# Performance work log

Hardware: AMD Instinct MI355X
Metric: run time of the kernel (lower is better)

The kernel has to match this reference:

```python
import jax, jax.numpy as jnp
import numpy as np

TOP_K = 2
NUM_EXPERTS = 8


def setup_inputs() -> dict:
    key = jax.random.key(0)
    ks = jax.random.split(key, 9)
    ob, ib, slen, dim, hidden, E = 1, 1, 2048, 2048, 1024, NUM_EXPERTS
    std = 0.02  # trunc_normal init std in the original module
    return {
        "x": jax.random.normal(ks[0], (ob, ib, slen, dim), dtype=jnp.float32),
        "gate": jax.random.normal(ks[1], (dim, E), dtype=jnp.float32) * std,
        "expert_bias": jnp.zeros((E,), dtype=jnp.float32),
        "w1": jax.random.normal(ks[2], (E, hidden, dim), dtype=jnp.float32) * std,
        "w2": jax.random.normal(ks[3], (E, dim, hidden), dtype=jnp.float32) * std,
        "w3": jax.random.normal(ks[4], (E, hidden, dim), dtype=jnp.float32) * std,
        "sw1": jax.random.normal(ks[5], (hidden, dim), dtype=jnp.float32) * std,
        "sw2": jax.random.normal(ks[6], (dim, hidden), dtype=jnp.float32) * std,
        "sw3": jax.random.normal(ks[7], (hidden, dim), dtype=jnp.float32) * std,
    }


def reference(x, gate, expert_bias, w1, w2, w3, sw1, sw2, sw3):
    ob, ib, slen, dim = x.shape
    E = w1.shape[0]
    xt = x.reshape(ob, ib * slen, dim)  # (ob, N, dim)

    # ---- router: sigmoid scores, top-k on (scores + expert_bias), gather raw scores ----
    logits = jnp.einsum('ond,de->one', xt, gate).astype(jnp.float32)
    scores = jax.nn.sigmoid(logits)                          # (ob, N, E)
    _, idx = jax.lax.top_k(scores + expert_bias, TOP_K)      # (ob, N, K) int32
    top_scores = jnp.take_along_axis(scores, idx, axis=2)    # route_norm=False, route_scale=1.0

    # combine weights: per-(token, expert) routing score (0 if not selected)
    cw = jnp.einsum('onke,onk->eon',
                    jax.nn.one_hot(idx, E, dtype=top_scores.dtype), top_scores)

    # ---- grouped experts (bf16 SwiGLU); score applied BEFORE experts ----
    # Matmul is linear, so silu(W1 @ (s*x)) == silu(s * (W1 @ x)); tokens with s=0 contribute 0.
    xb = xt.astype(jnp.bfloat16)
    s = cw[..., None].astype(jnp.bfloat16)                   # (E, ob, N, 1)
    g = jnp.einsum('ond,ehd->eonh', xb, w1.astype(jnp.bfloat16))
    u = jnp.einsum('ond,ehd->eonh', xb, w3.astype(jnp.bfloat16))
    h = jax.nn.silu(s * g) * (s * u)                         # (E, ob, N, hidden)
    routed = jnp.einsum('eonh,edh->ond', h, w2.astype(jnp.bfloat16)).astype(xt.dtype)

    # ---- shared expert (fp32 SwiGLU) ----
    hs = jax.nn.silu(jnp.einsum('ond,hd->onh', xt, sw1)) * jnp.einsum('ond,hd->onh', xt, sw3)
    shared = jnp.einsum('onh,dh->ond', hs, sw2)

    return (shared + routed).reshape(ob, ib, slen, dim)
```

## Files before the change

### kernel.cpp

```cpp
#include <hip/hip_runtime.h>

#define NTOK 2048
#define DIM  2048
#define HID  1024
#define NEXP 8
#define SHBASE 5120

typedef float f32x4 __attribute__((ext_vector_type(4)));
typedef __bf16 bf16x8 __attribute__((ext_vector_type(8)));

__device__ __forceinline__ unsigned int f2bf(float f) {
    unsigned int u = __float_as_uint(f);
    u += 0x7FFFu + ((u >> 16) & 1u);
    return u >> 16;
}
__device__ __forceinline__ float bf2f(unsigned int h) {
    return __uint_as_float(h << 16);
}
__device__ __forceinline__ int pack2(float a, float b) {
    return (int)(f2bf(a) | (f2bf(b) << 16));
}
__device__ __forceinline__ void gload16(const void* g, void* l) {
    __builtin_amdgcn_global_load_lds(
        (__attribute__((address_space(1))) void*)(g),
        (__attribute__((address_space(3))) void*)(l), 16, 0, 0);
}

__global__ __launch_bounds__(256) void cast_kernel(
    const float* __restrict__ src, unsigned short* __restrict__ dst, int n4)
{
    int i = blockIdx.x * 256 + threadIdx.x;
    if (i >= n4) return;
    float4 v = reinterpret_cast<const float4*>(src)[i];
    int2 o;
    o.x = pack2(v.x, v.y);
    o.y = pack2(v.z, v.w);
    reinterpret_cast<int2*>(dst)[i] = o;
}

__global__ __launch_bounds__(256) void router_kernel(
    const float* __restrict__ x, const float* __restrict__ gate,
    const float* __restrict__ bias, float* __restrict__ sc, int* __restrict__ top2)
{
    const int n = blockIdx.x;
    const int t = threadIdx.x;
    float acc[8];
#pragma unroll
    for (int e = 0; e < 8; ++e) acc[e] = 0.f;
    const float* xr = x + (size_t)n * DIM;
    for (int d = t; d < DIM; d += 256) {
        float xv = xr[d];
        float4 g0 = *reinterpret_cast<const float4*>(gate + d * 8);
        float4 g1 = *reinterpret_cast<const float4*>(gate + d * 8 + 4);
        acc[0] += xv * g0.x; acc[1] += xv * g0.y;
        acc[2] += xv * g0.z; acc[3] += xv * g0.w;
        acc[4] += xv * g1.x; acc[5] += xv * g1.y;
        acc[6] += xv * g1.z; acc[7] += xv * g1.w;
    }
#pragma unroll
    for (int e = 0; e < 8; ++e) {
#pragma unroll
        for (int off = 32; off > 0; off >>= 1)
            acc[e] += __shfl_down(acc[e], off, 64);
    }
    __shared__ float red[4][8];
    const int lane = t & 63, wv = t >> 6;
    if (lane == 0) {
#pragma unroll
        for (int e = 0; e < 8; ++e) red[wv][e] = acc[e];
    }
    __syncthreads();
    if (t == 0) {
        float scv[8];
#pragma unroll
        for (int e = 0; e < 8; ++e) {
            float v = red[0][e] + red[1][e] + red[2][e] + red[3][e];
            scv[e] = 1.f / (1.f + expf(-v));
        }
        int i1 = 0; float b1 = -1e30f;
#pragma unroll
        for (int e = 0; e < 8; ++e) { float b = scv[e] + bias[e]; if (b > b1) { b1 = b; i1 = e; } }
        int i2 = -1; float b2 = -1e30f;
#pragma unroll
        for (int e = 0; e < 8; ++e) { if (e == i1) continue; float b = scv[e] + bias[e]; if (b > b2) { b2 = b; i2 = e; } }
#pragma unroll
        for (int e = 0; e < 8; ++e) sc[n * 8 + e] = scv[e];
        top2[n * 2]     = i1;
        top2[n * 2 + 1] = i2;
    }
}

__global__ __launch_bounds__(256) void lists_kernel(
    const int* __restrict__ top2, int* __restrict__ gcnt, int* __restrict__ gbase,
    int* __restrict__ tid, int* __restrict__ rows)
{
    __shared__ int cnt[8], run[8], base[8];
    const int t = threadIdx.x;
    if (t < 8) { cnt[t] = 0; run[t] = 0; }
    __syncthreads();
    for (int tok = t; tok < NTOK; tok += 256) {
        atomicAdd(&cnt[top2[tok * 2]], 1);
        atomicAdd(&cnt[top2[tok * 2 + 1]], 1);
    }
    __syncthreads();
    if (t == 0) {
        int c = 0;
        for (int e = 0; e < 8; ++e) { base[e] = c; c += (cnt[e] + 127) & ~127; }
    }
    __syncthreads();
    for (int tok = t; tok < NTOK; tok += 256) {
#pragma unroll
        for (int k = 0; k < 2; ++k) {
            int e = top2[tok * 2 + k];
            int pos = atomicAdd(&run[e], 1);
            tid[e * NTOK + pos] = tok;
            rows[tok * 2 + k] = base[e] + pos;
        }
    }
    __syncthreads();
    if (t < 8) { gcnt[t] = cnt[t]; gbase[t] = base[t]; }
}

__global__ __launch_bounds__(256) void up_kernel(
    const unsigned short* __restrict__ xb,
    const unsigned short* __restrict__ w1b, const unsigned short* __restrict__ w3b,
    const unsigned short* __restrict__ sw1b, const unsigned short* __restrict__ sw3b,
    const float* __restrict__ sc, const int* __restrict__ gcnt, const int* __restrict__ gbase,
    const int* __restrict__ tid, unsigned short* __restrict__ h2g)
{
    const int e = blockIdx.z;
    int cnt, base;
    const unsigned short *w1e, *w3e;
    const int* tl = nullptr;
    if (e < NEXP) {
        cnt = gcnt[e];
        if ((int)blockIdx.x * 128 >= cnt) return;
        base = gbase[e];
        w1e = w1b + (size_t)e * HID * DIM;
        w3e = w3b + (size_t)e * HID * DIM;
        tl = tid + e * NTOK;
    } else {
        cnt = NTOK; base = SHBASE; w1e = sw1b; w3e = sw3b;
    }
    const int m0 = blockIdx.x * 128, n0 = blockIdx.y * 64;

    __shared__ char lA[16384];
    __shared__ char lB1[8192];
    __shared__ char lB2[8192];

    const int t = threadIdx.x;
    const int lane = t & 63, wv = t >> 6;
    const int wm = wv >> 1, wn = wv & 1;
    const int lr = lane & 15, hi = lane >> 4;
    const int srow = lane >> 3;
    const int scolb = (lane & 7) << 4;

    const char* aS[4]; char* aD[4];
#pragma unroll
    for (int p = 0; p < 4; ++p) {
        int r = p * 32 + wv * 8 + srow;
        int ridx = (e < NEXP) ? tl[min(m0 + r, cnt - 1)] : (m0 + r);
        aS[p] = (const char*)xb + (size_t)ridx * (DIM * 2) + (scolb ^ ((r & 7) << 4));
        aD[p] = lA + p * 4096 + wv * 1024;
    }
    const char *b1S[2], *b3S[2]; char *bD[2];
#pragma unroll
    for (int q = 0; q < 2; ++q) {
        int r = q * 32 + wv * 8 + srow;
        size_t ro = (size_t)(n0 + r) * (DIM * 2) + (scolb ^ ((r & 7) << 4));
        b1S[q] = (const char*)w1e + ro;
        b3S[q] = (const char*)w3e + ro;
        bD[q] = (char*)0 + q * 4096 + wv * 1024;
    }

    f32x4 accG[4][2], accU[4][2];
    const f32x4 zz = {0.f, 0.f, 0.f, 0.f};
#pragma unroll
    for (int m = 0; m < 4; ++m)
#pragma unroll
        for (int n = 0; n < 2; ++n) { accG[m][n] = zz; accU[m][n] = zz; }

    for (int kb = 0; kb < DIM * 2; kb += 128) {
#pragma unroll
        for (int p = 0; p < 4; ++p) gload16(aS[p] + kb, aD[p]);
#pragma unroll
        for (int q = 0; q < 2; ++q) {
            size_t off = q * 4096 + wv * 1024;
            gload16(b1S[q] + kb, lB1 + off);
            gload16(b3S[q] + kb, lB2 + off);
        }
        __syncthreads();
#pragma unroll
        for (int kk = 0; kk < 2; ++kk) {
            bf16x8 af[4], b1f[2], b2f[2];
            const int cb = kk * 64 + hi * 16;
#pragma unroll
            for (int m = 0; m < 4; ++m) {
                int row = wm * 64 + m * 16 + lr;
                af[m] = *reinterpret_cast<const bf16x8*>(lA + row * 128 + (cb ^ ((row & 7) << 4)));
            }
#pragma unroll
            for (int n = 0; n < 2; ++n) {
                int row = wn * 32 + n * 16 + lr;
                int off = row * 128 + (cb ^ ((row & 7) << 4));
                b1f[n] = *reinterpret_cast<const bf16x8*>(lB1 + off);
                b2f[n] = *reinterpret_cast<const bf16x8*>(lB2 + off);
            }
#pragma unroll
            for (int m = 0; m < 4; ++m)
#pragma unroll
                for (int n = 0; n < 2; ++n) {
                    accG[m][n] = __builtin_amdgcn_mfma_f32_16x16x32_bf16(af[m], b1f[n], accG[m][n], 0, 0, 0);
                    accU[m][n] = __builtin_amdgcn_mfma_f32_16x16x32_bf16(af[m], b2f[n], accU[m][n], 0, 0, 0);
                }
        }
        __syncthreads();
    }

#pragma unroll
    for (int m = 0; m < 4; ++m) {
#pragma unroll
        for (int r = 0; r < 4; ++r) {
            int row = wm * 64 + m * 16 + hi * 4 + r;
            float sv = 1.0f;
            if (e < NEXP) {
                int tok = tl[min(m0 + row, cnt - 1)];
                sv = sc[tok * NEXP + e];
            }
            unsigned short* hrow = h2g + (size_t)(base + m0 + row) * HID + n0;
#pragma unroll
            for (int n = 0; n < 2; ++n) {
                int col = wn * 32 + n * 16 + lr;
                float g = bf2f(f2bf(accG[m][n][r] * sv));
                float u = bf2f(f2bf(accU[m][n][r] * sv));
                float hval = (g / (1.f + __expf(-g))) * u;
                hrow[col] = (unsigned short)f2bf(hval);
            }
        }
    }
}

__global__ __launch_bounds__(256) void down_kernel(
    const unsigned short* __restrict__ h2g,
    const unsigned short* __restrict__ w2b, const unsigned short* __restrict__ sw2b,
    const int* __restrict__ gcnt, const int* __restrict__ gbase,
    unsigned short* __restrict__ rb, float* __restrict__ out)
{
    const int e = blockIdx.z;
    int cnt, base;
    const unsigned short* w2e;
    if (e < NEXP) {
        cnt = gcnt[e];
        if ((int)blockIdx.x * 128 >= cnt) return;
        base = gbase[e];
        w2e = w2b + (size_t)e * DIM * HID;
    } else {
        cnt = NTOK; base = SHBASE; w2e = sw2b;
    }
    const int m0 = blockIdx.x * 128, n0 = blockIdx.y * 128;

    __shared__ char lA[16384];
    __shared__ char lB[16384];

    const int t = threadIdx.x;
    const int lane = t & 63, wv = t >> 6;
    const int wm = wv >> 1, wn = wv & 1;
    const int lr = lane & 15, hi = lane >> 4;
    const int srow = lane >> 3;
    const int scolb = (lane & 7) << 4;

    const char* aS[4]; const char* bS[4];
#pragma unroll
    for (int p = 0; p < 4; ++p) {
        int r = p * 32 + wv * 8 + srow;
        aS[p] = (const char*)h2g + (size_t)(base + m0 + r) * (HID * 2) + (scolb ^ ((r & 7) << 4));
        bS[p] = (const char*)w2e + (size_t)(n0 + r) * (HID * 2) + (scolb ^ ((r & 7) << 4));
    }

    f32x4 acc[4][4];
    const f32x4 zz = {0.f, 0.f, 0.f, 0.f};
#pragma unroll
    for (int m = 0; m < 4; ++m)
#pragma unroll
        for (int n = 0; n < 4; ++n) acc[m][n] = zz;

    for (int kb = 0; kb < HID * 2; kb += 128) {
#pragma unroll
        for (int p = 0; p < 4; ++p) {
            size_t off = p * 4096 + wv * 1024;
            gload16(aS[p] + kb, lA + off);
            gload16(bS[p] + kb, lB + off);
        }
        __syncthreads();
#pragma unroll
        for (int kk = 0; kk < 2; ++kk) {
            bf16x8 af[4], bfr[4];
            const int cb = kk * 64 + hi * 16;
#pragma unroll
            for (int m = 0; m < 4; ++m) {
                int row = wm * 64 + m * 16 + lr;
                af[m] = *reinterpret_cast<const bf16x8*>(lA + row * 128 + (cb ^ ((row & 7) << 4)));
                int rowb = wn * 64 + m * 16 + lr;
                bfr[m] = *reinterpret_cast<const bf16x8*>(lB + rowb * 128 + (cb ^ ((rowb & 7) << 4)));
            }
#pragma unroll
            for (int m = 0; m < 4; ++m)
#pragma unroll
                for (int n = 0; n < 4; ++n)
                    acc[m][n] = __builtin_amdgcn_mfma_f32_16x16x32_bf16(af[m], bfr[n], acc[m][n], 0, 0, 0);
        }
        __syncthreads();
    }

#pragma unroll
    for (int m = 0; m < 4; ++m)
#pragma unroll
        for (int r = 0; r < 4; ++r) {
            int row = wm * 64 + m * 16 + hi * 4 + r;
            if (e < NEXP) {
                unsigned short* rrow = rb + (size_t)(base + m0 + row) * DIM + n0 + wn * 64;
#pragma unroll
                for (int n = 0; n < 4; ++n)
                    rrow[n * 16 + lr] = (unsigned short)f2bf(acc[m][n][r]);
            } else {
                float* orow = out + (size_t)(m0 + row) * DIM + n0 + wn * 64;
#pragma unroll
                for (int n = 0; n < 4; ++n)
                    orow[n * 16 + lr] = acc[m][n][r];
            }
        }
}

__global__ __launch_bounds__(256) void combine_kernel(
    const int* __restrict__ rows, const unsigned short* __restrict__ rb,
    float* __restrict__ out)
{
    int i = blockIdx.x * 256 + threadIdx.x;
    int tok = i >> 8, g = i & 255;
    int r1 = rows[tok * 2], r2 = rows[tok * 2 + 1];
    float4* op = reinterpret_cast<float4*>(out + (size_t)tok * DIM + g * 8);
    int4 a = *reinterpret_cast<const int4*>(rb + (size_t)r1 * DIM + g * 8);
    int4 b = *reinterpret_cast<const int4*>(rb + (size_t)r2 * DIM + g * 8);
    float4 o0 = op[0], o1 = op[1];
    o0.x += bf2f((unsigned)a.x & 0xFFFF) + bf2f((unsigned)b.x & 0xFFFF);
    o0.y += bf2f((unsigned)a.x >> 16)    + bf2f((unsigned)b.x >> 16);
    o0.z += bf2f((unsigned)a.y & 0xFFFF) + bf2f((unsigned)b.y & 0xFFFF);
    o0.w += bf2f((unsigned)a.y >> 16)    + bf2f((unsigned)b.y >> 16);
    o1.x += bf2f((unsigned)a.z & 0xFFFF) + bf2f((unsigned)b.z & 0xFFFF);
    o1.y += bf2f((unsigned)a.z >> 16)    + bf2f((unsigned)b.z >> 16);
    o1.z += bf2f((unsigned)a.w & 0xFFFF) + bf2f((unsigned)b.w & 0xFFFF);
    o1.w += bf2f((unsigned)a.w >> 16)    + bf2f((unsigned)b.w >> 16);
    op[0] = o0; op[1] = o1;
}

extern "C" void kernel_launch(void* const* d_in, const int* in_sizes, int n_in,
                              void* d_out, int out_size, void* d_ws, size_t ws_size,
                              hipStream_t stream) {
    const float* x    = (const float*)d_in[0];
    const float* gate = (const float*)d_in[1];
    const float* bias = (const float*)d_in[2];
    const float* w1   = (const float*)d_in[3];
    const float* w2   = (const float*)d_in[4];
    const float* w3   = (const float*)d_in[5];
    const float* sw1  = (const float*)d_in[6];
    const float* sw2  = (const float*)d_in[7];
    const float* sw3  = (const float*)d_in[8];
    float* out = (float*)d_out;

    char* ws = (char*)d_ws;
    size_t o = 0;
    unsigned short* xb   = (unsigned short*)(ws + o); o += 8388608;
    unsigned short* w1b  = (unsigned short*)(ws + o); o += 33554432;
    unsigned short* w3b  = (unsigned short*)(ws + o); o += 33554432;
    unsigned short* w2b  = (unsigned short*)(ws + o); o += 33554432;
    unsigned short* sw1b = (unsigned short*)(ws + o); o += 4194304;
    unsigned short* sw3b = (unsigned short*)(ws + o); o += 4194304;
    unsigned short* sw2b = (unsigned short*)(ws + o); o += 4194304;
    unsigned short* h2g  = (unsigned short*)(ws + o); o += 14680064;
    unsigned short* rb   = (unsigned short*)(ws + o); o += 20971520;
    float* sc            = (float*)(ws + o);          o += 65536;
    int* top2            = (int*)(ws + o);            o += 16384;
    int* tid             = (int*)(ws + o);            o += 65536;
    int* rows            = (int*)(ws + o);            o += 16384;
    int* gcnt            = (int*)(ws + o);            o += 256;
    int* gbase           = (int*)(ws + o);            o += 256;

    cast_kernel<<<4096,  256, 0, stream>>>(x,   xb,   1048576);
    cast_kernel<<<16384, 256, 0, stream>>>(w1,  w1b,  4194304);
    cast_kernel<<<16384, 256, 0, stream>>>(w3,  w3b,  4194304);
    cast_kernel<<<16384, 256, 0, stream>>>(w2,  w2b,  4194304);
    cast_kernel<<<2048,  256, 0, stream>>>(sw1, sw1b, 524288);
    cast_kernel<<<2048,  256, 0, stream>>>(sw3, sw3b, 524288);
    cast_kernel<<<2048,  256, 0, stream>>>(sw2, sw2b, 524288);
    router_kernel<<<2048, 256, 0, stream>>>(x, gate, bias, sc, top2);
    lists_kernel<<<1, 256, 0, stream>>>(top2, gcnt, gbase, tid, rows);
    up_kernel<<<dim3(16, 16, 9), 256, 0, stream>>>(xb, w1b, w3b, sw1b, sw3b, sc, gcnt, gbase, tid, h2g);
    down_kernel<<<dim3(16, 16, 9), 256, 0, stream>>>(h2g, w2b, sw2b, gcnt, gbase, rb, out);
    combine_kernel<<<2048, 256, 0, stream>>>(rows, rb, out);
}
```

Measured before the change: 601.4 us.

## Enlarge GEMM tiles to 256 rows with 512 threads and double-buffer LDS

The up and down expert GEMM kernels now use 256-row tiles with 512-thread blocks, and wider N tiles (128 for up, 256 for down). Each kernel keeps two 64 KB LDS buffers so the next K-slice is loaded while the current one is computed. Expert segments are padded to 256 rows, and workspace and the shared-expert base offset grow to match. The aim is more data reuse per tile and hiding global-load latency, at the cost of more padding waste per expert, more registers, and a 128 KB LDS footprint that limits occupancy to one block per CU.

```diff
diff --git a/kernel.cpp b/kernel.cpp
--- a/kernel.cpp
+++ b/kernel.cpp
@@ -4,7 +4,7 @@
 #define DIM  2048
 #define HID  1024
 #define NEXP 8
-#define SHBASE 5120
+#define SHBASE 6144
 
 typedef float f32x4 __attribute__((ext_vector_type(4)));
 typedef __bf16 bf16x8 __attribute__((ext_vector_type(8)));
@@ -25,6 +25,7 @@
         (__attribute__((address_space(1))) void*)(g),
         (__attribute__((address_space(3))) void*)(l), 16, 0, 0);
 }
+#define MFMA __builtin_amdgcn_mfma_f32_16x16x32_bf16
 
 __global__ __launch_bounds__(256) void cast_kernel(
     const float* __restrict__ src, unsigned short* __restrict__ dst, int n4)
@@ -105,7 +106,7 @@
     __syncthreads();
     if (t == 0) {
         int c = 0;
-        for (int e = 0; e < 8; ++e) { base[e] = c; c += (cnt[e] + 127) & ~127; }
+        for (int e = 0; e < 8; ++e) { base[e] = c; c += (cnt[e] + 255) & ~255; }
     }
     __syncthreads();
     for (int tok = t; tok < NTOK; tok += 256) {
@@ -121,7 +122,7 @@
     if (t < 8) { gcnt[t] = cnt[t]; gbase[t] = base[t]; }
 }
 
-__global__ __launch_bounds__(256) void up_kernel(
+__global__ __launch_bounds__(512) void up_kernel(
     const unsigned short* __restrict__ xb,
     const unsigned short* __restrict__ w1b, const unsigned short* __restrict__ w3b,
     const unsigned short* __restrict__ sw1b, const unsigned short* __restrict__ sw3b,
@@ -134,7 +135,7 @@
     const int* tl = nullptr;
     if (e < NEXP) {
         cnt = gcnt[e];
-        if ((int)blockIdx.x * 128 >= cnt) return;
+        if ((int)blockIdx.x * 256 >= cnt) return;
         base = gbase[e];
         w1e = w1b + (size_t)e * HID * DIM;
         w3e = w3b + (size_t)e * HID * DIM;
@@ -142,79 +143,84 @@
     } else {
         cnt = NTOK; base = SHBASE; w1e = sw1b; w3e = sw3b;
     }
-    const int m0 = blockIdx.x * 128, n0 = blockIdx.y * 64;
-
-    __shared__ char lA[16384];
-    __shared__ char lB1[8192];
-    __shared__ char lB2[8192];
+    const int m0 = blockIdx.x * 256, n0 = blockIdx.y * 128;
+
+    __shared__ char lds[131072];
 
     const int t = threadIdx.x;
     const int lane = t & 63, wv = t >> 6;
     const int wm = wv >> 1, wn = wv & 1;
     const int lr = lane & 15, hi = lane >> 4;
-    const int srow = lane >> 3;
-    const int scolb = (lane & 7) << 4;
-
-    const char* aS[4]; char* aD[4];
+
+    const int scol = ((t & 7) << 4);
+    const char* aS[4];
 #pragma unroll
     for (int p = 0; p < 4; ++p) {
-        int r = p * 32 + wv * 8 + srow;
+        int r = p * 64 + (t >> 3);
         int ridx = (e < NEXP) ? tl[min(m0 + r, cnt - 1)] : (m0 + r);
-        aS[p] = (const char*)xb + (size_t)ridx * (DIM * 2) + (scolb ^ ((r & 7) << 4));
-        aD[p] = lA + p * 4096 + wv * 1024;
-    }
-    const char *b1S[2], *b3S[2]; char *bD[2];
-#pragma unroll
-    for (int q = 0; q < 2; ++q) {
-        int r = q * 32 + wv * 8 + srow;
-        size_t ro = (size_t)(n0 + r) * (DIM * 2) + (scolb ^ ((r & 7) << 4));
-        b1S[q] = (const char*)w1e + ro;
-        b3S[q] = (const char*)w3e + ro;
-        bD[q] = (char*)0 + q * 4096 + wv * 1024;
-    }
-
-    f32x4 accG[4][2], accU[4][2];
+        aS[p] = (const char*)xb + (size_t)ridx * (DIM * 2) + (scol ^ ((r & 7) << 4));
+    }
+    const char *b1S[2], *b3S[2];
+#pragma unroll
+    for (int p = 0; p < 2; ++p) {
+        int r = p * 64 + (t >> 3);
+        size_t ro = (size_t)(n0 + r) * (DIM * 2) + (scol ^ ((r & 7) << 4));
+        b1S[p] = (const char*)w1e + ro;
+        b3S[p] = (const char*)w3e + ro;
+    }
+
+    f32x4 accG[4][4], accU[4][4];
     const f32x4 zz = {0.f, 0.f, 0.f, 0.f};
 #pragma unroll
     for (int m = 0; m < 4; ++m)
 #pragma unroll
-        for (int n = 0; n < 2; ++n) { accG[m][n] = zz; accU[m][n] = zz; }
-
-    for (int kb = 0; kb < DIM * 2; kb += 128) {
-#pragma unroll
-        for (int p = 0; p < 4; ++p) gload16(aS[p] + kb, aD[p]);
-#pragma unroll
-        for (int q = 0; q < 2; ++q) {
-            size_t off = q * 4096 + wv * 1024;
-            gload16(b1S[q] + kb, lB1 + off);
-            gload16(b3S[q] + kb, lB2 + off);
-        }
-        __syncthreads();
+        for (int n = 0; n < 4; ++n) { accG[m][n] = zz; accU[m][n] = zz; }
+
+    auto STAGE = [&](int bo, int kb) {
+#pragma unroll
+        for (int p = 0; p < 4; ++p)
+            gload16(aS[p] + kb, lds + bo + p * 8192 + wv * 1024);
+#pragma unroll
+        for (int p = 0; p < 2; ++p) {
+            gload16(b1S[p] + kb, lds + bo + 32768 + p * 8192 + wv * 1024);
+            gload16(b3S[p] + kb, lds + bo + 49152 + p * 8192 + wv * 1024);
+        }
+    };
+
+    int bo = 0;
+    STAGE(0, 0);
+    __syncthreads();
+    for (int it = 0; it < 32; ++it) {
+        if (it < 31) STAGE(bo ^ 65536, (it + 1) * 128);
+        const char* A  = lds + bo;
+        const char* B1 = A + 32768;
+        const char* B2 = A + 49152;
 #pragma unroll
         for (int kk = 0; kk < 2; ++kk) {
-            bf16x8 af[4], b1f[2], b2f[2];
+            bf16x8 af[4], b1f[4], b2f[4];
             const int cb = kk * 64 + hi * 16;
 #pragma unroll
             for (int m = 0; m < 4; ++m) {
                 int row = wm * 64 + m * 16 + lr;
-                af[m] = *reinterpret_cast<const bf16x8*>(lA + row * 128 + (cb ^ ((row & 7) << 4)));
-            }
-#pragma unroll
-            for (int n = 0; n < 2; ++n) {
-                int row = wn * 32 + n * 16 + lr;
+                af[m] = *reinterpret_cast<const bf16x8*>(A + row * 128 + (cb ^ ((row & 7) << 4)));
+            }
+#pragma unroll
+            for (int n = 0; n < 4; ++n) {
+                int row = wn * 64 + n * 16 + lr;
                 int off = row * 128 + (cb ^ ((row & 7) << 4));
-                b1f[n] = *reinterpret_cast<const bf16x8*>(lB1 + off);
-                b2f[n] = *reinterpret_cast<const bf16x8*>(lB2 + off);
+                b1f[n] = *reinterpret_cast<const bf16x8*>(B1 + off);
+                b2f[n] = *reinterpret_cast<const bf16x8*>(B2 + off);
             }
 #pragma unroll
             for (int m = 0; m < 4; ++m)
 #pragma unroll
-                for (int n = 0; n < 2; ++n) {
-                    accG[m][n] = __builtin_amdgcn_mfma_f32_16x16x32_bf16(af[m], b1f[n], accG[m][n], 0, 0, 0);
-                    accU[m][n] = __builtin_amdgcn_mfma_f32_16x16x32_bf16(af[m], b2f[n], accU[m][n], 0, 0, 0);
+                for (int n = 0; n < 4; ++n) {
+                    accG[m][n] = MFMA(af[m], b1f[n], accG[m][n], 0, 0, 0);
+                    accU[m][n] = MFMA(af[m], b2f[n], accU[m][n], 0, 0, 0);
                 }
         }
         __syncthreads();
+        bo ^= 65536;
     }
 
 #pragma unroll
@@ -223,24 +229,20 @@
         for (int r = 0; r < 4; ++r) {
             int row = wm * 64 + m * 16 + hi * 4 + r;
             float sv = 1.0f;
-            if (e < NEXP) {
-                int tok = tl[min(m0 + row, cnt - 1)];
-                sv = sc[tok * NEXP + e];
-            }
+            if (e < NEXP) sv = sc[tl[min(m0 + row, cnt - 1)] * NEXP + e];
             unsigned short* hrow = h2g + (size_t)(base + m0 + row) * HID + n0;
 #pragma unroll
-            for (int n = 0; n < 2; ++n) {
-                int col = wn * 32 + n * 16 + lr;
+            for (int n = 0; n < 4; ++n) {
+                int col = wn * 64 + n * 16 + lr;
                 float g = bf2f(f2bf(accG[m][n][r] * sv));
                 float u = bf2f(f2bf(accU[m][n][r] * sv));
-                float hval = (g / (1.f + __expf(-g))) * u;
-                hrow[col] = (unsigned short)f2bf(hval);
-            }
-        }
-    }
-}
-
-__global__ __launch_bounds__(256) void down_kernel(
+                hrow[col] = (unsigned short)f2bf((g / (1.f + __expf(-g))) * u);
+            }
+        }
+    }
+}
+
+__global__ __launch_bounds__(512) void down_kernel(
     const unsigned short* __restrict__ h2g,
     const unsigned short* __restrict__ w2b, const unsigned short* __restrict__ sw2b,
     const int* __restrict__ gcnt, const int* __restrict__ gbase,
@@ -251,72 +253,81 @@
     const unsigned short* w2e;
     if (e < NEXP) {
         cnt = gcnt[e];
-        if ((int)blockIdx.x * 128 >= cnt) return;
+        if ((int)blockIdx.x * 256 >= cnt) return;
         base = gbase[e];
         w2e = w2b + (size_t)e * DIM * HID;
     } else {
         cnt = NTOK; base = SHBASE; w2e = sw2b;
     }
-    const int m0 = blockIdx.x * 128, n0 = blockIdx.y * 128;
-
-    __shared__ char lA[16384];
-    __shared__ char lB[16384];
+    const int m0 = blockIdx.x * 256, n0 = blockIdx.y * 256;
+
+    __shared__ char lds[131072];
 
     const int t = threadIdx.x;
     const int lane = t & 63, wv = t >> 6;
-    const int wm = wv >> 1, wn = wv & 1;
+    const int wm = wv >> 2, wn = wv & 3;
     const int lr = lane & 15, hi = lane >> 4;
-    const int srow = lane >> 3;
-    const int scolb = (lane & 7) << 4;
-
+
+    const int scol = ((t & 7) << 4);
     const char* aS[4]; const char* bS[4];
 #pragma unroll
     for (int p = 0; p < 4; ++p) {
-        int r = p * 32 + wv * 8 + srow;
-        aS[p] = (const char*)h2g + (size_t)(base + m0 + r) * (HID * 2) + (scolb ^ ((r & 7) << 4));
-        bS[p] = (const char*)w2e + (size_t)(n0 + r) * (HID * 2) + (scolb ^ ((r & 7) << 4));
-    }
-
-    f32x4 acc[4][4];
+        int r = p * 64 + (t >> 3);
+        aS[p] = (const char*)h2g + (size_t)(base + m0 + r) * (HID * 2) + (scol ^ ((r & 7) << 4));
+        bS[p] = (const char*)w2e + (size_t)(n0 + r) * (HID * 2) + (scol ^ ((r & 7) << 4));
+    }
+
+    f32x4 acc[8][4];
     const f32x4 zz = {0.f, 0.f, 0.f, 0.f};
 #pragma unroll
-    for (int m = 0; m < 4; ++m)
+    for (int m = 0; m < 8; ++m)
 #pragma unroll
         for (int n = 0; n < 4; ++n) acc[m][n] = zz;
 
-    for (int kb = 0; kb < HID * 2; kb += 128) {
+    auto STAGE = [&](int bo, int kb) {
 #pragma unroll
         for (int p = 0; p < 4; ++p) {
-            size_t off = p * 4096 + wv * 1024;
-            gload16(aS[p] + kb, lA + off);
-            gload16(bS[p] + kb, lB + off);
+            gload16(aS[p] + kb, lds + bo + p * 8192 + wv * 1024);
+            gload16(bS[p] + kb, lds + bo + 32768 + p * 8192 + wv * 1024);
+        }
+    };
+
+    int bo = 0;
+    STAGE(0, 0);
+    __syncthreads();
+    for (int it = 0; it < 16; ++it) {
+        if (it < 15) STAGE(bo ^ 65536, (it + 1) * 128);
+        const char* A = lds + bo;
+        const char* B = A + 32768;
+#pragma unroll
+        for (int kk = 0; kk < 2; ++kk) {
+            bf16x8 af[8], bfr[4];
+            const int cb = kk * 64 + hi * 16;
+#pragma unroll
+            for (int m = 0; m < 8; ++m) {
+                int row = wm * 128 + m * 16 + lr;
+                af[m] = *reinterpret_cast<const bf16x8*>(A + row * 128 + (cb ^ ((row & 7) << 4)));
+            }
+#pragma unroll
+            for (int n = 0; n < 4; ++n) {
+                int row = wn * 64 + n * 16 + lr;
+                bfr[n] = *reinterpret_cast<const bf16x8*>(B + row * 128 + (cb ^ ((row & 7) << 4)));
+            }
+#pragma unroll
+            for (int m = 0; m < 8; ++m)
+#pragma unroll
+                for (int n = 0; n < 4; ++n)
+                    acc[m][n] = MFMA(af[m], bfr[n], acc[m][n], 0, 0, 0);
         }
         __syncthreads();
-#pragma unroll
-        for (int kk = 0; kk < 2; ++kk) {
-            bf16x8 af[4], bfr[4];
-            const int cb = kk * 64 + hi * 16;
-#pragma unroll
-            for (int m = 0; m < 4; ++m) {
-                int row = wm * 64 + m * 16 + lr;
-                af[m] = *reinterpret_cast<const bf16x8*>(lA + row * 128 + (cb ^ ((row & 7) << 4)));
-                int rowb = wn * 64 + m * 16 + lr;
-                bfr[m] = *reinterpret_cast<const bf16x8*>(lB + rowb * 128 + (cb ^ ((rowb & 7) << 4)));
-            }
-#pragma unroll
-            for (int m = 0; m < 4; ++m)
-#pragma unroll
-                for (int n = 0; n < 4; ++n)
-                    acc[m][n] = __builtin_amdgcn_mfma_f32_16x16x32_bf16(af[m], bfr[n], acc[m][n], 0, 0, 0);
-        }
-        __syncthreads();
-    }
-
-#pragma unroll
-    for (int m = 0; m < 4; ++m)
+        bo ^= 65536;
+    }
+
+#pragma unroll
+    for (int m = 0; m < 8; ++m)
 #pragma unroll
         for (int r = 0; r < 4; ++r) {
-            int row = wm * 64 + m * 16 + hi * 4 + r;
+            int row = wm * 128 + m * 16 + hi * 4 + r;
             if (e < NEXP) {
                 unsigned short* rrow = rb + (size_t)(base + m0 + row) * DIM + n0 + wn * 64;
 #pragma unroll
@@ -376,8 +387,8 @@
     unsigned short* sw1b = (unsigned short*)(ws + o); o += 4194304;
     unsigned short* sw3b = (unsigned short*)(ws + o); o += 4194304;
     unsigned short* sw2b = (unsigned short*)(ws + o); o += 4194304;
-    unsigned short* h2g  = (unsigned short*)(ws + o); o += 14680064;
-    unsigned short* rb   = (unsigned short*)(ws + o); o += 20971520;
+    unsigned short* h2g  = (unsigned short*)(ws + o); o += 16777216;
+    unsigned short* rb   = (unsigned short*)(ws + o); o += 25165824;
     float* sc            = (float*)(ws + o);          o += 65536;
     int* top2            = (int*)(ws + o);            o += 16384;
     int* tid             = (int*)(ws + o);            o += 65536;
@@ -394,7 +405,7 @@
     cast_kernel<<<2048,  256, 0, stream>>>(sw2, sw2b, 524288);
     router_kernel<<<2048, 256, 0, stream>>>(x, gate, bias, sc, top2);
     lists_kernel<<<1, 256, 0, stream>>>(top2, gcnt, gbase, tid, rows);
-    up_kernel<<<dim3(16, 16, 9), 256, 0, stream>>>(xb, w1b, w3b, sw1b, sw3b, sc, gcnt, gbase, tid, h2g);
-    down_kernel<<<dim3(16, 16, 9), 256, 0, stream>>>(h2g, w2b, sw2b, gcnt, gbase, rb, out);
+    up_kernel<<<dim3(8, 8, 9), 512, 0, stream>>>(xb, w1b, w3b, sw1b, sw3b, sc, gcnt, gbase, tid, h2g);
+    down_kernel<<<dim3(8, 8, 9), 512, 0, stream>>>(h2g, w2b, sw2b, gcnt, gbase, rb, out);
     combine_kernel<<<2048, 256, 0, stream>>>(rows, rb, out);
 }
```

Result: faster. 535.4 us (-11.0%).
